# Kernel tuning notes

Hardware: AMD Instinct MI355X
Metric: run time of the kernel (lower is better)

Reference implementation:

```python
import jax, jax.numpy as jnp
import numpy as np

B, V, T, F, H = 32, 16, 64, 64, 512
NBINS = 36  # 360 / delta (delta_cog = delta_rb = 10)
OUT = 4     # output_size


def setup_inputs() -> dict:
    key = jax.random.key(0)
    ks = jax.random.split(key, 12)
    s = 1.0 / np.sqrt(H)
    return {
        'sequence': jax.random.normal(ks[0], (B, V, T, F), jnp.float32),
        'dist_matrix': jax.random.uniform(ks[1], (B, V, T, V), jnp.float32),
        'rb_matrix': jax.random.randint(ks[2], (B, V, T, V), 0, NBINS).astype(jnp.int32),
        'cog_matrix': jax.random.randint(ks[3], (B, V, T, V), 0, NBINS).astype(jnp.int32),
        'seq_mask': jnp.ones((B, V, T), jnp.float32),
        'maxval': jax.random.uniform(ks[4], (B, F), jnp.float32) + 1.0,
        'minval': jax.random.uniform(ks[5], (B, F), jnp.float32),
        # per-vessel LSTMCell params (PyTorch gate order i,f,g,o stacked along 4H)
        'W_ih': jax.random.normal(ks[6], (V, 4 * H, F), jnp.float32) * s,
        'W_hh': jax.random.normal(ks[7], (V, 4 * H, H), jnp.float32) * s,
        'b_ih': jnp.zeros((V, 4 * H), jnp.float32),
        'b_hh': jnp.zeros((V, 4 * H), jnp.float32),
        # hardwired attention domain table [360/delta_cog, 360/delta_rb]
        'domain': jax.random.normal(ks[8], (NBINS, NBINS), jnp.float32),
        # per-vessel softAttention linear (2H -> H)
        'soft_W': jax.random.normal(ks[9], (V, H, 2 * H), jnp.float32) * s,
        'soft_b': jnp.zeros((V, H), jnp.float32),
        # shared output linear (H -> F)
        'out_W': jax.random.normal(ks[10], (F, H), jnp.float32) * s,
        'out_b': jnp.zeros((F,), jnp.float32),
    }


def _forward(sequence, dist_matrix, rb_matrix, cog_matrix, seq_mask, maxval, minval,
             W_ih, W_hh, b_ih, b_hh, domain, soft_W, soft_b, out_W, out_b):
    B_, V_, T_, F_ = sequence.shape
    H_ = W_hh.shape[-1]

    def hardwired(h, r, d, m, cg):
        # h: [B,V,H]; r,d,cg: [B,V,V]; m: [B,V]
        mul1 = m[:, :, None] * m[:, None, :]
        mul2 = domain[cg, r]
        w = jax.nn.relu(mul2 - d) * mul1
        w = w / jax.lax.stop_gradient(jnp.max(w))  # torch: weights /= weights.data.max()
        return jnp.einsum('bvw,bwh->bvh', w, h)

    def lstm_step(x, h, c):
        # vectorized over V independent LSTMCells
        g = (jnp.einsum('bvf,vgf->bvg', x, W_ih)
             + jnp.einsum('bvh,vgh->bvg', h, W_hh) + b_ih + b_hh)
        i, f, gg, o = jnp.split(g, 4, axis=-1)
        c_new = jax.nn.sigmoid(f) * c + jax.nn.sigmoid(i) * jnp.tanh(gg)
        h_new = jax.nn.sigmoid(o) * jnp.tanh(c_new)
        return h_new, c_new

    h0 = jnp.zeros((B_, V_, H_), sequence.dtype)
    c0 = jnp.zeros((B_, V_, H_), sequence.dtype)
    xs = (jnp.moveaxis(sequence, 2, 0), jnp.moveaxis(rb_matrix, 2, 0),
          jnp.moveaxis(dist_matrix, 2, 0), jnp.moveaxis(seq_mask, 2, 0),
          jnp.moveaxis(cog_matrix, 2, 0))

    def enc_step(carry, xt):
        h, c = carry
        x, r, d, m, cg = xt
        wh = hardwired(h, r, d, m, cg)
        h, c = lstm_step(x, wh, c)
        return (h, c), h

    (h, c), enc = jax.lax.scan(enc_step, (h0, c0), xs)
    enc = jnp.moveaxis(enc, 0, 2)  # encodedInput [B,V,T,H]

    # decoder, prediction step i=0 (prediction_length=1)
    wh = hardwired(h, rb_matrix[:, :, -1], dist_matrix[:, :, -1],
                   seq_mask[:, :, -1], cog_matrix[:, :, -1])
    # get_previous_sequence: denormalize under no_grad
    prev = jax.lax.stop_gradient(
        sequence[:, :, -1] * (maxval - minval)[:, None, :] + minval[:, None, :])
    h, c = lstm_step(prev, wh, c)

    # per-vessel softAttention
    score = jnp.einsum('bvth,bvh->bvt', enc, h)
    alpha = jax.nn.softmax(score * seq_mask, axis=-1)
    ctx = jnp.einsum('bvt,bvth->bvh', alpha, enc)
    # faithful to torch.stack((ctx, h)).view(B, 2H) memory-reinterpret per vessel
    z = jnp.moveaxis(jnp.stack([ctx, h], axis=0), 2, 0).reshape(V_, B_, 2 * H_)
    h = jnp.moveaxis(
        jnp.tanh(jnp.einsum('vbk,vhk->vbh', z, soft_W) + soft_b[:, None, :]), 0, 1)

    out = jax.nn.relu(jnp.einsum('bvh,fh->bvf', h, out_W) + out_b)
    return out[:, :, None, :OUT]  # [B, V, prediction_length=1, output_size]


def reference(sequence, dist_matrix, rb_matrix, cog_matrix, seq_mask, maxval, minval,
              W_ih, W_hh, b_ih, b_hh, domain, soft_W, soft_b, out_W, out_b,
              maxVessels=V):
    return _forward(sequence, dist_matrix, rb_matrix, cog_matrix, seq_mask,
                    maxval, minval, W_ih, W_hh, b_ih, b_hh, domain,
                    soft_W, soft_b, out_W, out_b)
```

## Files before the change

### kernel.cpp

```cpp
#include <hip/hip_runtime.h>
#include <math.h>

#define B 32
#define V 16
#define T 64
#define F 64
#define H 512
#define NB 36
#define G4H 2048

typedef unsigned short u16;
typedef unsigned long long ull;
typedef __attribute__((ext_vector_type(8))) short bf16x8;
typedef __attribute__((ext_vector_type(4))) float f32x4;

#define OFF_H0     0
#define OFF_H1     262144
#define OFF_C      524288
#define OFF_CNT    786432
#define OFF_WALL   819200
#define OFF_CTX    819200
#define OFF_HSOFT  1081344
#define OFF_WMAX   1343488
#define OFF_WHSTG  1343552
#define OFF_SEQSTG 1605696
#define OFF_WSTG   2670656
#define OFF_ENC    12107840

#define WHP 262144
#define WLDS_BYTES 147456

__device__ __forceinline__ float sigmoidf_(float x) { return 1.0f / (1.0f + __expf(-x)); }

__device__ __forceinline__ u16 f2bf(float f) {
    union { float f; unsigned u; } x; x.f = f;
    unsigned r = x.u + 0x7FFF + ((x.u >> 16) & 1);
    return (u16)(r >> 16);
}
__device__ __forceinline__ float bf2f(u16 u) {
    union { unsigned i; float f; } x; x.i = ((unsigned)u) << 16;
    return x.f;
}
__device__ __forceinline__ f32x4 mfma16(bf16x8 a, bf16x8 b, f32x4 c) {
    return __builtin_amdgcn_mfma_f32_16x16x32_bf16(a, b, c, 0, 0, 0);
}
__device__ __forceinline__ bf16x8 mk_bf16x8(ull lo, ull hi) {
    union { ull u[2]; bf16x8 v; } x; x.u[0] = lo; x.u[1] = hi; return x.v;
}
__device__ __forceinline__ bf16x8 mk_bf16x8q(uint4 q) {
    union { uint4 q; bf16x8 v; } x; x.q = q; return x.v;
}

__device__ __forceinline__ ull ld_agent(const ull* p) {
    return __hip_atomic_load((ull*)p, __ATOMIC_RELAXED, __HIP_MEMORY_SCOPE_AGENT);
}
__device__ __forceinline__ void st_agent(ull* p, ull x) {
    __hip_atomic_store(p, x, __ATOMIC_RELAXED, __HIP_MEMORY_SCOPE_AGENT);
}
__device__ __forceinline__ void st_agent_f(float* p, float x) {
    __hip_atomic_store(p, x, __ATOMIC_RELAXED, __HIP_MEMORY_SCOPE_AGENT);
}
__device__ __forceinline__ void st_agent_u32(unsigned* p, unsigned x) {
    __hip_atomic_store(p, x, __ATOMIC_RELAXED, __HIP_MEMORY_SCOPE_AGENT);
}
__device__ __forceinline__ unsigned ld_agent_u32(const unsigned* p) {
    return __hip_atomic_load((unsigned*)p, __ATOMIC_RELAXED, __HIP_MEMORY_SCOPE_AGENT);
}

#define NZB 3200
#define NHW 64
#define NWC 4608
#define NSS 1040
__global__ __launch_bounds__(256) void k_prep(
    float* __restrict__ ws,
    const float* __restrict__ dist, const int* __restrict__ rb,
    const int* __restrict__ cog, const float* __restrict__ mask,
    const float* __restrict__ domain, float* __restrict__ w_all,
    float* __restrict__ wmax_all,
    const float* __restrict__ W_ih, const float* __restrict__ W_hh,
    u16* __restrict__ Wstg,
    const float* __restrict__ seq, const float* __restrict__ maxval,
    const float* __restrict__ minval, u16* __restrict__ seqstg) {
    __shared__ float red[256];
    int bid = blockIdx.x;
    int tid = threadIdx.x;

    if (bid < NZB) {
        ws[bid * 256 + tid] = 0.0f;
        return;
    }
    if (bid < NZB + NHW) {
        int t = bid - NZB;
        float lmax = 0.0f;
        for (int idx = tid; idx < B * V * V; idx += 256) {
            int b = idx >> 8;
            int rem = idx & 255;
            int i = rem >> 4, j = rem & 15;
            int base = ((b * V + i) * T + t) * V + j;
            float val = domain[cog[base] * NB + rb[base]] - dist[base];
            val = val > 0.0f ? val : 0.0f;
            val *= mask[(b * V + i) * T + t] * mask[(b * V + j) * T + t];
            w_all[t * (B * V * V) + idx] = val;
            lmax = fmaxf(lmax, val);
        }
        red[tid] = lmax;
        __syncthreads();
        for (int s = 128; s > 0; s >>= 1) {
            if (tid < s) red[tid] = fmaxf(red[tid], red[tid + s]);
            __syncthreads();
        }
        if (tid == 0) wmax_all[t] = red[0];
        return;
    }
    if (bid < NZB + NHW + NWC) {
        int idx = bid - (NZB + NHW);
        int v = idx / 288, hk = (idx / 18) & 15, ks = idx % 18;
#pragma unroll
        for (int s = 0; s < 2; ++s) {
            int slot = tid + s * 256;
            int nt = slot >> 6, lane = slot & 63;
            int g = nt >> 1, hh = nt & 1;
            int col = g * H + hk * 32 + hh * 16 + (lane & 15);
            int k = ks * 32 + ((lane >> 4) << 3);
            const float* src = (k < F) ? &W_ih[(v * G4H + col) * F + k]
                                       : &W_hh[(v * G4H + col) * H + (k - F)];
            float4 x0 = *(const float4*)src;
            float4 x1 = *(const float4*)(src + 4);
            union { u16 u[8]; uint4 q; } pk;
            pk.u[0] = f2bf(x0.x); pk.u[1] = f2bf(x0.y); pk.u[2] = f2bf(x0.z); pk.u[3] = f2bf(x0.w);
            pk.u[4] = f2bf(x1.x); pk.u[5] = f2bf(x1.y); pk.u[6] = f2bf(x1.z); pk.u[7] = f2bf(x1.w);
            *(uint4*)&Wstg[(size_t)((((v * 16 + hk) * 18 + ks) * 8 + nt) * 64 + lane) * 8] = pk.q;
        }
        return;
    }
    {
        int idx = bid - (NZB + NHW + NWC);
        int v = idx / 65, t = idx % 65;
        int mt = tid >> 7, ks = (tid >> 6) & 1, lane = tid & 63;
        int b = mt * 16 + (lane & 15);
        int f = ks * 32 + ((lane >> 4) << 3);
        union { u16 u[8]; uint4 q; } pk;
        if (t < T) {
            const float* sp = &seq[((b * V + v) * T + t) * F + f];
            float4 x0 = *(const float4*)sp, x1 = *(const float4*)(sp + 4);
            pk.u[0] = f2bf(x0.x); pk.u[1] = f2bf(x0.y); pk.u[2] = f2bf(x0.z); pk.u[3] = f2bf(x0.w);
            pk.u[4] = f2bf(x1.x); pk.u[5] = f2bf(x1.y); pk.u[6] = f2bf(x1.z); pk.u[7] = f2bf(x1.w);
        } else {
            const float* sp = &seq[((b * V + v) * T + (T - 1)) * F + f];
            float4 x0 = *(const float4*)sp, x1 = *(const float4*)(sp + 4);
            float4 mx0 = *(const float4*)&maxval[b * F + f], mx1 = *(const float4*)&maxval[b * F + f + 4];
            float4 mn0 = *(const float4*)&minval[b * F + f], mn1 = *(const float4*)&minval[b * F + f + 4];
            pk.u[0] = f2bf(x0.x * (mx0.x - mn0.x) + mn0.x);
            pk.u[1] = f2bf(x0.y * (mx0.y - mn0.y) + mn0.y);
            pk.u[2] = f2bf(x0.z * (mx0.z - mn0.z) + mn0.z);
            pk.u[3] = f2bf(x0.w * (mx0.w - mn0.w) + mn0.w);
            pk.u[4] = f2bf(x1.x * (mx1.x - mn1.x) + mn1.x);
            pk.u[5] = f2bf(x1.y * (mx1.y - mn1.y) + mn1.y);
            pk.u[6] = f2bf(x1.z * (mx1.z - mn1.z) + mn1.z);
            pk.u[7] = f2bf(x1.w * (mx1.w - mn1.w) + mn1.w);
        }
        *(uint4*)&seqstg[(((size_t)(t * 16 + v)) * 4 + mt * 2 + ks) * 512 + lane * 8] = pk.q;
    }
}

__global__ __launch_bounds__(256) void k_recur(
    const u16* __restrict__ seqstg, const u16* __restrict__ Wstg,
    const float* __restrict__ w_all, const float* __restrict__ wmax_all,
    const float* __restrict__ b_ih, const float* __restrict__ b_hh,
    float* __restrict__ h0buf, float* __restrict__ h1buf,
    float* __restrict__ c, u16* __restrict__ enc, u16* __restrict__ whstg,
    unsigned* __restrict__ bar) {
    extern __shared__ u16 Wlds[];

    int bid = blockIdx.x;
    int v = bid & 15, hk = bid >> 4;
    int tid = threadIdx.x;

    {
        const uint4* wsrc = (const uint4*)(Wstg + (size_t)((v * 16 + hk) * 18) * 4096);
        uint4* wdst = (uint4*)Wlds;
        for (int i = tid; i < 9216; i += 256) wdst[i] = wsrc[i];
    }

    int lane = tid & 63, wvi = tid >> 6;
    int mtw = wvi & 1, hh = wvi >> 1;
    int col = hk * 32 + hh * 16 + (lane & 15);
    int q4 = (lane >> 4) << 2;
    float bi = b_ih[v * G4H + col] + b_hh[v * G4H + col];
    float bf_ = b_ih[v * G4H + H + col] + b_hh[v * G4H + H + col];
    float bg_ = b_ih[v * G4H + 2 * H + col] + b_hh[v * G4H + 2 * H + col];
    float bo = b_ih[v * G4H + 3 * H + col] + b_hh[v * G4H + 3 * H + col];

    unsigned* aslot = bar + (v * 16 + hk) * 16;
    unsigned* bslot = bar + (256 + hk * 16 + v) * 16;
    unsigned* apoll = bar + (v * 16 + (tid & 15)) * 16;
    unsigned* bpoll = bar + (256 + hk * 16 + (tid & 15)) * 16;

    int a_b = tid >> 3;
    int a_cq = tid & 7;
    const int wh_idx = ((((v * 2 + (a_b >> 4)) * 16 + hk) * 64 +
                         (((a_cq >> 1) << 4) + (a_b & 15))) * 8 + (a_cq & 1) * 4);

    __syncthreads();

    for (int t = 0; t <= T; ++t) {
        int par = t & 1;
        int tm = t < T ? t : (T - 1);
        const float* hin = (t & 1) ? h0buf : h1buf;
        float* hout = (t & 1) ? h1buf : h0buf;

        uint4 s0 = *(const uint4*)&seqstg[(((size_t)(t * 16 + v)) * 4 + mtw * 2 + 0) * 512 + lane * 8];
        uint4 s1 = *(const uint4*)&seqstg[(((size_t)(t * 16 + v)) * 4 + mtw * 2 + 1) * 512 + lane * 8];
        float inv = 1.0f / wmax_all[tm];
        const float* wrow = &w_all[(size_t)tm * (B * V * V) + (a_b * V + v) * V];
        float4 wr0 = *(const float4*)(wrow);
        float4 wr1 = *(const float4*)(wrow + 4);
        float4 wr2 = *(const float4*)(wrow + 8);
        float4 wr3 = *(const float4*)(wrow + 12);
        float cprev[4];
#pragma unroll
        for (int r = 0; r < 4; ++r)
            cprev[r] = c[((mtw * 16 + q4 + r) * V + v) * H + col];

        f32x4 acc[4];
        acc[0][0] = bi;  acc[0][1] = bi;  acc[0][2] = bi;  acc[0][3] = bi;
        acc[1][0] = bf_; acc[1][1] = bf_; acc[1][2] = bf_; acc[1][3] = bf_;
        acc[2][0] = bg_; acc[2][1] = bg_; acc[2][2] = bg_; acc[2][3] = bg_;
        acc[3][0] = bo;  acc[3][1] = bo;  acc[3][2] = bo;  acc[3][3] = bo;
        {
            bf16x8 a0f = mk_bf16x8q(s0);
            bf16x8 a1f = mk_bf16x8q(s1);
#pragma unroll
            for (int g = 0; g < 4; ++g)
                acc[g] = mfma16(a0f, *(const bf16x8*)&Wlds[(0 * 8 + (g * 2 + hh)) * 512 + lane * 8], acc[g]);
#pragma unroll
            for (int g = 0; g < 4; ++g)
                acc[g] = mfma16(a1f, *(const bf16x8*)&Wlds[(1 * 8 + (g * 2 + hh)) * 512 + lane * 8], acc[g]);
        }

        if (t > 0) {
            if (tid < 16) {
                while (ld_agent_u32(bpoll) < (unsigned)t) __builtin_amdgcn_s_sleep(1);
            }
            __syncthreads();
        }

        {
            const ull* hb = (const ull*)&hin[(a_b * V) * H + hk * 32 + a_cq * 4];
            float a0 = 0.f, a1 = 0.f, a2 = 0.f, a3 = 0.f;
            const float wj[16] = {wr0.x, wr0.y, wr0.z, wr0.w, wr1.x, wr1.y, wr1.z, wr1.w,
                                  wr2.x, wr2.y, wr2.z, wr2.w, wr3.x, wr3.y, wr3.z, wr3.w};
#pragma unroll
            for (int j = 0; j < 16; ++j) {
                ull lo = ld_agent(hb + (size_t)j * (H / 2));
                ull hi = ld_agent(hb + (size_t)j * (H / 2) + 1);
                union { ull u; float f[2]; } u0, u1;
                u0.u = lo; u1.u = hi;
                a0 = fmaf(wj[j], u0.f[0], a0);
                a1 = fmaf(wj[j], u0.f[1], a1);
                a2 = fmaf(wj[j], u1.f[0], a2);
                a3 = fmaf(wj[j], u1.f[1], a3);
            }
            union { u16 u[4]; ull q; } pk;
            pk.u[0] = f2bf(a0 * inv); pk.u[1] = f2bf(a1 * inv);
            pk.u[2] = f2bf(a2 * inv); pk.u[3] = f2bf(a3 * inv);
            st_agent((ull*)&whstg[par * WHP + wh_idx], pk.q);
        }
        __syncthreads();
        if (tid == 0) st_agent_u32(aslot, (unsigned)(t + 1));

        if (tid < 16) {
            while (ld_agent_u32(apoll) < (unsigned)(t + 1)) __builtin_amdgcn_s_sleep(1);
        }
        __syncthreads();

        bf16x8 afr[16];
#pragma unroll
        for (int ksw = 0; ksw < 16; ++ksw) {
            const ull* src = (const ull*)&whstg[par * WHP + (((v * 2 + mtw) * 16 + ksw) * 64 + lane) * 8];
            ull lo = ld_agent(src), hi = ld_agent(src + 1);
            afr[ksw] = mk_bf16x8(lo, hi);
        }
#pragma unroll
        for (int ks = 0; ks < 16; ++ks) {
#pragma unroll
            for (int g = 0; g < 4; ++g) {
                bf16x8 wfr = *(const bf16x8*)&Wlds[((ks + 2) * 8 + (g * 2 + hh)) * 512 + lane * 8];
                acc[g] = mfma16(afr[ks], wfr, acc[g]);
            }
        }

        float cnv[4], hnv[4];
#pragma unroll
        for (int r = 0; r < 4; ++r) {
            float gi = acc[0][r];
            float gf = acc[1][r];
            float gg = acc[2][r];
            float go = acc[3][r];
            cnv[r] = sigmoidf_(gf) * cprev[r] + sigmoidf_(gi) * tanhf(gg);
            hnv[r] = sigmoidf_(go) * tanhf(cnv[r]);
            int b = mtw * 16 + q4 + r;
            st_agent_f(&hout[(b * V + v) * H + col], hnv[r]);
        }
        if (t < T) {
            __syncthreads();
            if (tid == 0) st_agent_u32(bslot, (unsigned)(t + 1));
        }

#pragma unroll
        for (int r = 0; r < 4; ++r) {
            int b = mtw * 16 + q4 + r;
            c[(b * V + v) * H + col] = cnv[r];
            if (t < T) enc[((size_t)(b * V + v) * T + t) * H + col] = f2bf(hnv[r]);
        }
    }
}

__global__ __launch_bounds__(256) void k_attn(
    const u16* __restrict__ enc, const float* __restrict__ h,
    const float* __restrict__ mask, float* __restrict__ ctx) {
    int bid = blockIdx.x;
    int b = bid >> 4, v = bid & 15;
    int tid = threadIdx.x;
    int wave = tid >> 6, lane = tid & 63;
    __shared__ float hs[H];
    __shared__ float sc[T];
    __shared__ float al[T];
    const u16* encbase = enc + (size_t)((b * V + v) * T) * H;
    const float* hb = h + (b * V + v) * H;
    for (int i = tid; i < H; i += 256) hs[i] = hb[i];
    __syncthreads();
    for (int tt = wave; tt < T; tt += 4) {
        const u16* e = encbase + tt * H;
        float p = 0.0f;
#pragma unroll
        for (int ii = 0; ii < 8; ++ii) p += bf2f(e[ii * 64 + lane]) * hs[ii * 64 + lane];
        for (int off = 32; off; off >>= 1) p += __shfl_down(p, off, 64);
        if (lane == 0) sc[tt] = p;
    }
    __syncthreads();
    if (tid < 64) {
        float m_t = mask[(b * V + v) * T + tid];
        float s = sc[tid] * m_t;
        float mx = s;
        for (int off = 32; off; off >>= 1) mx = fmaxf(mx, __shfl_xor(mx, off, 64));
        float e = __expf(s - mx);
        float sum = e;
        for (int off = 32; off; off >>= 1) sum += __shfl_xor(sum, off, 64);
        al[tid] = e / sum;
    }
    __syncthreads();
    for (int hh = tid; hh < H; hh += 256) {
        float a = 0.0f;
        for (int tt = 0; tt < T; ++tt) a += al[tt] * bf2f(encbase[tt * H + hh]);
        ctx[(b * V + v) * H + hh] = a;
    }
}

__global__ __launch_bounds__(256) void k_soft(
    const float* __restrict__ ctx, const float* __restrict__ hdec,
    const float* __restrict__ soft_W, const float* __restrict__ soft_b,
    float* __restrict__ hsoft) {
    int v = blockIdx.x;
    int h0 = blockIdx.y * 32;
    int tid = threadIdx.x;
    int cg = tid & 31, rg = tid >> 5;
    __shared__ float sA[32][36];
    __shared__ float sW2[32][36];
    float* sAf = &sA[0][0];
    float* sWf = &sW2[0][0];
    float acc[4] = {0.f, 0.f, 0.f, 0.f};
    int arow = tid >> 3, akq = tid & 7;
    float4 areg, wreg;

    {
        int k = akq * 4;
        const float* src = (arow < 16) ? ctx : hdec;
        int bsrc = 2 * (arow & 15) + (k >= H ? 1 : 0);
        areg = *(const float4*)&src[(bsrc * V + v) * H + (k & (H - 1))];
        wreg = *(const float4*)&soft_W[(v * H + h0 + arow) * (2 * H) + k];
    }
    for (int kc = 0; kc < 2 * H; kc += 32) {
        __syncthreads();
        *(float4*)&sAf[arow * 36 + akq * 4] = areg;
        *(float4*)&sWf[arow * 36 + akq * 4] = wreg;
        __syncthreads();
        if (kc + 32 < 2 * H) {
            int k = kc + 32 + akq * 4;
            const float* src = (arow < 16) ? ctx : hdec;
            int bsrc = 2 * (arow & 15) + (k >= H ? 1 : 0);
            areg = *(const float4*)&src[(bsrc * V + v) * H + (k & (H - 1))];
            wreg = *(const float4*)&soft_W[(v * H + h0 + arow) * (2 * H) + kc + 32 + akq * 4];
        }
#pragma unroll
        for (int k4 = 0; k4 < 8; ++k4) {
            float4 wv = *(const float4*)&sWf[cg * 36 + k4 * 4];
            float4 a0 = *(const float4*)&sAf[(rg * 4 + 0) * 36 + k4 * 4];
            float4 a1 = *(const float4*)&sAf[(rg * 4 + 1) * 36 + k4 * 4];
            float4 a2 = *(const float4*)&sAf[(rg * 4 + 2) * 36 + k4 * 4];
            float4 a3 = *(const float4*)&sAf[(rg * 4 + 3) * 36 + k4 * 4];
            acc[0] += a0.x * wv.x + a0.y * wv.y + a0.z * wv.z + a0.w * wv.w;
            acc[1] += a1.x * wv.x + a1.y * wv.y + a1.z * wv.z + a1.w * wv.w;
            acc[2] += a2.x * wv.x + a2.y * wv.y + a2.z * wv.z + a2.w * wv.w;
            acc[3] += a3.x * wv.x + a3.y * wv.y + a3.z * wv.z + a3.w * wv.w;
        }
    }
    float bb = soft_b[v * H + h0 + cg];
#pragma unroll
    for (int r = 0; r < 4; ++r) {
        int row = rg * 4 + r;
        hsoft[(row * V + v) * H + h0 + cg] = tanhf(acc[r] + bb);
    }
}

__global__ __launch_bounds__(64) void k_out(
    const float* __restrict__ hsoft, const float* __restrict__ outW,
    const float* __restrict__ outb, float* __restrict__ out) {
    int bid = blockIdx.x;
    int b = bid >> 4, v = bid & 15;
    int lane = threadIdx.x;
    const float* hb = hsoft + (b * V + v) * H;
    float p[4] = {0.0f, 0.0f, 0.0f, 0.0f};
#pragma unroll
    for (int ii = 0; ii < 8; ++ii) {
        float hv = hb[ii * 64 + lane];
#pragma unroll
        for (int o = 0; o < 4; ++o) p[o] += hv * outW[o * H + ii * 64 + lane];
    }
#pragma unroll
    for (int o = 0; o < 4; ++o) {
        float s = p[o];
        for (int off = 32; off; off >>= 1) s += __shfl_down(s, off, 64);
        if (lane == 0) {
            float val = s + outb[o];
            out[(b * V + v) * 4 + o] = val > 0.0f ? val : 0.0f;
        }
    }
}

extern "C" void kernel_launch(void* const* d_in, const int* in_sizes, int n_in,
                              void* d_out, int out_size, void* d_ws, size_t ws_size,
                              hipStream_t stream) {
    const float* seq = (const float*)d_in[0];
    const float* dist = (const float*)d_in[1];
    const int* rb = (const int*)d_in[2];
    const int* cog = (const int*)d_in[3];
    const float* mask = (const float*)d_in[4];
    const float* maxval = (const float*)d_in[5];
    const float* minval = (const float*)d_in[6];
    const float* W_ih = (const float*)d_in[7];
    const float* W_hh = (const float*)d_in[8];
    const float* b_ih = (const float*)d_in[9];
    const float* b_hh = (const float*)d_in[10];
    const float* domain = (const float*)d_in[11];
    const float* soft_W = (const float*)d_in[12];
    const float* soft_b = (const float*)d_in[13];
    const float* out_W = (const float*)d_in[14];
    const float* out_b = (const float*)d_in[15];

    float* ws = (float*)d_ws;
    float* h0buf = ws + OFF_H0;
    float* h1buf = ws + OFF_H1;
    float* c = ws + OFF_C;
    unsigned* bar = (unsigned*)(ws + OFF_CNT);
    float* w_all = ws + OFF_WALL;
    float* ctx = ws + OFF_CTX;
    float* hsoft = ws + OFF_HSOFT;
    float* wmax_all = ws + OFF_WMAX;
    u16* whstg = (u16*)(ws + OFF_WHSTG);
    u16* seqstg = (u16*)(ws + OFF_SEQSTG);
    u16* Wstg = (u16*)(ws + OFF_WSTG);
    u16* enc = (u16*)(ws + OFF_ENC);

    (void)hipFuncSetAttribute((const void*)k_recur,
                              hipFuncAttributeMaxDynamicSharedMemorySize, WLDS_BYTES);

    k_prep<<<NZB + NHW + NWC + NSS, 256, 0, stream>>>(
        ws, dist, rb, cog, mask, domain, w_all, wmax_all,
        W_ih, W_hh, Wstg, seq, maxval, minval, seqstg);

    k_recur<<<256, 256, WLDS_BYTES, stream>>>(seqstg, Wstg, w_all, wmax_all,
                                              b_ih, b_hh, h0buf, h1buf, c, enc,
                                              whstg, bar);

    k_attn<<<B * V, 256, 0, stream>>>(enc, h0buf, mask, ctx);
    k_soft<<<dim3(16, 16), 256, 0, stream>>>(ctx, h0buf, soft_W, soft_b, hsoft);
    k_out<<<B * V, 64, 0, stream>>>(hsoft, out_W, out_b, (float*)d_out);
}
```

Before: 700.8 us.

## Fuse attention, soft-attention linear and output head into persistent recurrent kernel

Merges the attention, softAttention linear and output-projection kernels into the persistent recurrence kernel. Flag-based grid barriers in workspace replace the kernel boundaries, and agent-scope atomic loads and stores make cross-block data visible. This removes three launches and their tail gaps. It adds spin waits, and the enc writes become 16-bit atomic stores, which may cost bandwidth in the recurrence loop.

```diff
diff --git a/kernel.cpp b/kernel.cpp
--- a/kernel.cpp
+++ b/kernel.cpp
@@ -58,6 +58,9 @@
     __hip_atomic_store(p, x, __ATOMIC_RELAXED, __HIP_MEMORY_SCOPE_AGENT);
 }
 __device__ __forceinline__ void st_agent_f(float* p, float x) {
+    __hip_atomic_store(p, x, __ATOMIC_RELAXED, __HIP_MEMORY_SCOPE_AGENT);
+}
+__device__ __forceinline__ void st_agent_u16(u16* p, u16 x) {
     __hip_atomic_store(p, x, __ATOMIC_RELAXED, __HIP_MEMORY_SCOPE_AGENT);
 }
 __device__ __forceinline__ void st_agent_u32(unsigned* p, unsigned x) {
@@ -163,14 +166,22 @@
     }
 }
 
-__global__ __launch_bounds__(256) void k_recur(
+__global__ __launch_bounds__(256) void k_main(
     const u16* __restrict__ seqstg, const u16* __restrict__ Wstg,
     const float* __restrict__ w_all, const float* __restrict__ wmax_all,
     const float* __restrict__ b_ih, const float* __restrict__ b_hh,
     float* __restrict__ h0buf, float* __restrict__ h1buf,
     float* __restrict__ c, u16* __restrict__ enc, u16* __restrict__ whstg,
-    unsigned* __restrict__ bar) {
+    unsigned* __restrict__ bar,
+    const float* __restrict__ mask, const float* __restrict__ soft_W,
+    const float* __restrict__ soft_b, const float* __restrict__ out_W,
+    const float* __restrict__ out_b, float* __restrict__ ctx,
+    float* __restrict__ hsoft, float* __restrict__ out) {
     extern __shared__ u16 Wlds[];
+    __shared__ float hs[H];
+    __shared__ float scal[2 * T];
+    __shared__ float sA[32][36];
+    __shared__ float sW2[32][36];
 
     int bid = blockIdx.x;
     int v = bid & 15, hk = bid >> 4;
@@ -311,129 +322,169 @@
         for (int r = 0; r < 4; ++r) {
             int b = mtw * 16 + q4 + r;
             c[(b * V + v) * H + col] = cnv[r];
-            if (t < T) enc[((size_t)(b * V + v) * T + t) * H + col] = f2bf(hnv[r]);
-        }
-    }
-}
-
-__global__ __launch_bounds__(256) void k_attn(
-    const u16* __restrict__ enc, const float* __restrict__ h,
-    const float* __restrict__ mask, float* __restrict__ ctx) {
-    int bid = blockIdx.x;
-    int b = bid >> 4, v = bid & 15;
-    int tid = threadIdx.x;
-    int wave = tid >> 6, lane = tid & 63;
-    __shared__ float hs[H];
-    __shared__ float sc[T];
-    __shared__ float al[T];
-    const u16* encbase = enc + (size_t)((b * V + v) * T) * H;
-    const float* hb = h + (b * V + v) * H;
-    for (int i = tid; i < H; i += 256) hs[i] = hb[i];
+            if (t < T) st_agent_u16(&enc[((size_t)(b * V + v) * T + t) * H + col], f2bf(hnv[r]));
+        }
+    }
+
     __syncthreads();
-    for (int tt = wave; tt < T; tt += 4) {
-        const u16* e = encbase + tt * H;
-        float p = 0.0f;
-#pragma unroll
-        for (int ii = 0; ii < 8; ++ii) p += bf2f(e[ii * 64 + lane]) * hs[ii * 64 + lane];
-        for (int off = 32; off; off >>= 1) p += __shfl_down(p, off, 64);
-        if (lane == 0) sc[tt] = p;
+    if (tid == 0) st_agent_u32(bar + (512 + bid) * 16, 1u);
+    {
+        const unsigned* rs = bar + (512 + tid) * 16;
+        while (ld_agent_u32(rs) < 1u) __builtin_amdgcn_s_sleep(1);
     }
     __syncthreads();
-    if (tid < 64) {
-        float m_t = mask[(b * V + v) * T + tid];
-        float s = sc[tid] * m_t;
-        float mx = s;
-        for (int off = 32; off; off >>= 1) mx = fmaxf(mx, __shfl_xor(mx, off, 64));
-        float e = __expf(s - mx);
-        float sum = e;
-        for (int off = 32; off; off >>= 1) sum += __shfl_xor(sum, off, 64);
-        al[tid] = e / sum;
+
+    for (int u = 0; u < 2; ++u) {
+        int ab = (bid >> 4) + u * 16;
+        int av = bid & 15;
+        const u16* encb = enc + ((size_t)(ab * V + av) * T) * H;
+        {
+            ull x = ld_agent((const ull*)(h0buf + (ab * V + av) * H) + tid);
+            union { ull u; float f[2]; } q; q.u = x;
+            hs[tid * 2] = q.f[0]; hs[tid * 2 + 1] = q.f[1];
+        }
+        __syncthreads();
+        for (int tt = wvi; tt < T; tt += 4) {
+            const ull* ep = (const ull*)(encb + tt * H + lane * 8);
+            ull lo = ld_agent(ep), hi = ld_agent(ep + 1);
+            union { ull u; u16 s[4]; } x0, x1; x0.u = lo; x1.u = hi;
+            const float* hq = &hs[lane * 8];
+            float p = bf2f(x0.s[0]) * hq[0] + bf2f(x0.s[1]) * hq[1]
+                    + bf2f(x0.s[2]) * hq[2] + bf2f(x0.s[3]) * hq[3]
+                    + bf2f(x1.s[0]) * hq[4] + bf2f(x1.s[1]) * hq[5]
+                    + bf2f(x1.s[2]) * hq[6] + bf2f(x1.s[3]) * hq[7];
+            for (int off = 32; off; off >>= 1) p += __shfl_down(p, off, 64);
+            if (lane == 0) scal[tt] = p;
+        }
+        __syncthreads();
+        if (tid < 64) {
+            float m_t = mask[(ab * V + av) * T + tid];
+            float s = scal[tid] * m_t;
+            float mx = s;
+            for (int off = 32; off; off >>= 1) mx = fmaxf(mx, __shfl_xor(mx, off, 64));
+            float e = __expf(s - mx);
+            float sum = e;
+            for (int off = 32; off; off >>= 1) sum += __shfl_xor(sum, off, 64);
+            scal[T + tid] = e / sum;
+        }
+        __syncthreads();
+        if (tid < 128) {
+            float a0 = 0.f, a1 = 0.f, a2 = 0.f, a3 = 0.f;
+            for (int tt = 0; tt < T; ++tt) {
+                ull x = ld_agent((const ull*)(encb + tt * H + tid * 4));
+                union { ull u; u16 s[4]; } q; q.u = x;
+                float al = scal[T + tt];
+                a0 = fmaf(al, bf2f(q.s[0]), a0);
+                a1 = fmaf(al, bf2f(q.s[1]), a1);
+                a2 = fmaf(al, bf2f(q.s[2]), a2);
+                a3 = fmaf(al, bf2f(q.s[3]), a3);
+            }
+            float* cp = ctx + (ab * V + av) * H + tid * 4;
+            union { float f[2]; ull u; } q0, q1;
+            q0.f[0] = a0; q0.f[1] = a1; q1.f[0] = a2; q1.f[1] = a3;
+            st_agent((ull*)cp, q0.u);
+            st_agent((ull*)cp + 1, q1.u);
+        }
+        __syncthreads();
     }
     __syncthreads();
-    for (int hh = tid; hh < H; hh += 256) {
-        float a = 0.0f;
-        for (int tt = 0; tt < T; ++tt) a += al[tt] * bf2f(encbase[tt * H + hh]);
-        ctx[(b * V + v) * H + hh] = a;
-    }
-}
-
-__global__ __launch_bounds__(256) void k_soft(
-    const float* __restrict__ ctx, const float* __restrict__ hdec,
-    const float* __restrict__ soft_W, const float* __restrict__ soft_b,
-    float* __restrict__ hsoft) {
-    int v = blockIdx.x;
-    int h0 = blockIdx.y * 32;
-    int tid = threadIdx.x;
-    int cg = tid & 31, rg = tid >> 5;
-    __shared__ float sA[32][36];
-    __shared__ float sW2[32][36];
-    float* sAf = &sA[0][0];
-    float* sWf = &sW2[0][0];
-    float acc[4] = {0.f, 0.f, 0.f, 0.f};
-    int arow = tid >> 3, akq = tid & 7;
-    float4 areg, wreg;
+    if (tid == 0) st_agent_u32(bar + (768 + bid) * 16, 1u);
 
     {
-        int k = akq * 4;
-        const float* src = (arow < 16) ? ctx : hdec;
-        int bsrc = 2 * (arow & 15) + (k >= H ? 1 : 0);
-        areg = *(const float4*)&src[(bsrc * V + v) * H + (k & (H - 1))];
-        wreg = *(const float4*)&soft_W[(v * H + h0 + arow) * (2 * H) + k];
-    }
-    for (int kc = 0; kc < 2 * H; kc += 32) {
-        __syncthreads();
-        *(float4*)&sAf[arow * 36 + akq * 4] = areg;
-        *(float4*)&sWf[arow * 36 + akq * 4] = wreg;
-        __syncthreads();
-        if (kc + 32 < 2 * H) {
-            int k = kc + 32 + akq * 4;
-            const float* src = (arow < 16) ? ctx : hdec;
+        int sv = bid & 15;
+        int h0 = (bid >> 4) * 32;
+        if (tid < 16) {
+            const unsigned* cs = bar + (768 + tid * 16 + sv) * 16;
+            while (ld_agent_u32(cs) < 1u) __builtin_amdgcn_s_sleep(1);
+        }
+        __syncthreads();
+
+        int cg = tid & 31, rg = tid >> 5;
+        float* sAf = &sA[0][0];
+        float* sWf = &sW2[0][0];
+        float accs[4] = {0.f, 0.f, 0.f, 0.f};
+        int arow = tid >> 3, akq = tid & 7;
+        float4 areg, wreg;
+        {
+            int k = akq * 4;
+            const float* src = (arow < 16) ? ctx : h0buf;
             int bsrc = 2 * (arow & 15) + (k >= H ? 1 : 0);
-            areg = *(const float4*)&src[(bsrc * V + v) * H + (k & (H - 1))];
-            wreg = *(const float4*)&soft_W[(v * H + h0 + arow) * (2 * H) + kc + 32 + akq * 4];
-        }
-#pragma unroll
-        for (int k4 = 0; k4 < 8; ++k4) {
-            float4 wv = *(const float4*)&sWf[cg * 36 + k4 * 4];
-            float4 a0 = *(const float4*)&sAf[(rg * 4 + 0) * 36 + k4 * 4];
-            float4 a1 = *(const float4*)&sAf[(rg * 4 + 1) * 36 + k4 * 4];
-            float4 a2 = *(const float4*)&sAf[(rg * 4 + 2) * 36 + k4 * 4];
-            float4 a3 = *(const float4*)&sAf[(rg * 4 + 3) * 36 + k4 * 4];
-            acc[0] += a0.x * wv.x + a0.y * wv.y + a0.z * wv.z + a0.w * wv.w;
-            acc[1] += a1.x * wv.x + a1.y * wv.y + a1.z * wv.z + a1.w * wv.w;
-            acc[2] += a2.x * wv.x + a2.y * wv.y + a2.z * wv.z + a2.w * wv.w;
-            acc[3] += a3.x * wv.x + a3.y * wv.y + a3.z * wv.z + a3.w * wv.w;
-        }
-    }
-    float bb = soft_b[v * H + h0 + cg];
-#pragma unroll
-    for (int r = 0; r < 4; ++r) {
-        int row = rg * 4 + r;
-        hsoft[(row * V + v) * H + h0 + cg] = tanhf(acc[r] + bb);
-    }
-}
-
-__global__ __launch_bounds__(64) void k_out(
-    const float* __restrict__ hsoft, const float* __restrict__ outW,
-    const float* __restrict__ outb, float* __restrict__ out) {
-    int bid = blockIdx.x;
-    int b = bid >> 4, v = bid & 15;
-    int lane = threadIdx.x;
-    const float* hb = hsoft + (b * V + v) * H;
-    float p[4] = {0.0f, 0.0f, 0.0f, 0.0f};
-#pragma unroll
-    for (int ii = 0; ii < 8; ++ii) {
-        float hv = hb[ii * 64 + lane];
-#pragma unroll
-        for (int o = 0; o < 4; ++o) p[o] += hv * outW[o * H + ii * 64 + lane];
-    }
-#pragma unroll
-    for (int o = 0; o < 4; ++o) {
-        float s = p[o];
-        for (int off = 32; off; off >>= 1) s += __shfl_down(s, off, 64);
-        if (lane == 0) {
-            float val = s + outb[o];
-            out[(b * V + v) * 4 + o] = val > 0.0f ? val : 0.0f;
+            const float* sp = &src[(bsrc * V + sv) * H + (k & (H - 1))];
+            ull l0 = ld_agent((const ull*)sp), l1 = ld_agent((const ull*)sp + 1);
+            union { ull u[2]; float4 f; } q; q.u[0] = l0; q.u[1] = l1;
+            areg = q.f;
+            wreg = *(const float4*)&soft_W[(sv * H + h0 + arow) * (2 * H) + k];
+        }
+        for (int kc = 0; kc < 2 * H; kc += 32) {
+            __syncthreads();
+            *(float4*)&sAf[arow * 36 + akq * 4] = areg;
+            *(float4*)&sWf[arow * 36 + akq * 4] = wreg;
+            __syncthreads();
+            if (kc + 32 < 2 * H) {
+                int k = kc + 32 + akq * 4;
+                const float* src = (arow < 16) ? ctx : h0buf;
+                int bsrc = 2 * (arow & 15) + (k >= H ? 1 : 0);
+                const float* sp = &src[(bsrc * V + sv) * H + (k & (H - 1))];
+                ull l0 = ld_agent((const ull*)sp), l1 = ld_agent((const ull*)sp + 1);
+                union { ull u[2]; float4 f; } q; q.u[0] = l0; q.u[1] = l1;
+                areg = q.f;
+                wreg = *(const float4*)&soft_W[(sv * H + h0 + arow) * (2 * H) + kc + 32 + akq * 4];
+            }
+#pragma unroll
+            for (int k4 = 0; k4 < 8; ++k4) {
+                float4 wv = *(const float4*)&sWf[cg * 36 + k4 * 4];
+                float4 a0 = *(const float4*)&sAf[(rg * 4 + 0) * 36 + k4 * 4];
+                float4 a1 = *(const float4*)&sAf[(rg * 4 + 1) * 36 + k4 * 4];
+                float4 a2 = *(const float4*)&sAf[(rg * 4 + 2) * 36 + k4 * 4];
+                float4 a3 = *(const float4*)&sAf[(rg * 4 + 3) * 36 + k4 * 4];
+                accs[0] += a0.x * wv.x + a0.y * wv.y + a0.z * wv.z + a0.w * wv.w;
+                accs[1] += a1.x * wv.x + a1.y * wv.y + a1.z * wv.z + a1.w * wv.w;
+                accs[2] += a2.x * wv.x + a2.y * wv.y + a2.z * wv.z + a2.w * wv.w;
+                accs[3] += a3.x * wv.x + a3.y * wv.y + a3.z * wv.z + a3.w * wv.w;
+            }
+        }
+        float bb = soft_b[sv * H + h0 + cg];
+#pragma unroll
+        for (int r = 0; r < 4; ++r) {
+            int row = rg * 4 + r;
+            st_agent_f(&hsoft[(row * V + sv) * H + h0 + cg], tanhf(accs[r] + bb));
+        }
+    }
+    __syncthreads();
+    if (tid == 0) st_agent_u32(bar + (1024 + bid) * 16, 1u);
+
+    {
+        int ov = bid & 15;
+        if (tid < 16) {
+            const unsigned* ss = bar + (1024 + tid * 16 + ov) * 16;
+            while (ld_agent_u32(ss) < 1u) __builtin_amdgcn_s_sleep(1);
+        }
+        __syncthreads();
+        if (wvi < 2) {
+            int ob = (bid >> 4) + wvi * 16;
+            const float* hbp = hsoft + (ob * V + ov) * H + lane * 8;
+            ull q0 = ld_agent((const ull*)hbp);
+            ull q1 = ld_agent((const ull*)hbp + 1);
+            ull q2 = ld_agent((const ull*)hbp + 2);
+            ull q3 = ld_agent((const ull*)hbp + 3);
+            union { ull u[4]; float f[8]; } hv;
+            hv.u[0] = q0; hv.u[1] = q1; hv.u[2] = q2; hv.u[3] = q3;
+            float p[4] = {0.f, 0.f, 0.f, 0.f};
+#pragma unroll
+            for (int o = 0; o < 4; ++o) {
+                const float* wp = &out_W[o * H + lane * 8];
+#pragma unroll
+                for (int j = 0; j < 8; ++j) p[o] += hv.f[j] * wp[j];
+            }
+#pragma unroll
+            for (int o = 0; o < 4; ++o) {
+                float s = p[o];
+                for (int off = 32; off; off >>= 1) s += __shfl_down(s, off, 64);
+                if (lane == 0) {
+                    float val = s + out_b[o];
+                    out[(ob * V + ov) * 4 + o] = val > 0.0f ? val : 0.0f;
+                }
+            }
         }
     }
 }
@@ -472,18 +523,16 @@
     u16* Wstg = (u16*)(ws + OFF_WSTG);
     u16* enc = (u16*)(ws + OFF_ENC);
 
-    (void)hipFuncSetAttribute((const void*)k_recur,
+    (void)hipFuncSetAttribute((const void*)k_main,
                               hipFuncAttributeMaxDynamicSharedMemorySize, WLDS_BYTES);
 
     k_prep<<<NZB + NHW + NWC + NSS, 256, 0, stream>>>(
         ws, dist, rb, cog, mask, domain, w_all, wmax_all,
         W_ih, W_hh, Wstg, seq, maxval, minval, seqstg);
 
-    k_recur<<<256, 256, WLDS_BYTES, stream>>>(seqstg, Wstg, w_all, wmax_all,
-                                              b_ih, b_hh, h0buf, h1buf, c, enc,
-                                              whstg, bar);
-
-    k_attn<<<B * V, 256, 0, stream>>>(enc, h0buf, mask, ctx);
-    k_soft<<<dim3(16, 16), 256, 0, stream>>>(ctx, h0buf, soft_W, soft_b, hsoft);
-    k_out<<<B * V, 64, 0, stream>>>(hsoft, out_W, out_b, (float*)d_out);
-}
+    k_main<<<256, 256, WLDS_BYTES, stream>>>(seqstg, Wstg, w_all, wmax_all,
+                                             b_ih, b_hh, h0buf, h1buf, c, enc,
+                                             whstg, bar, mask, soft_W, soft_b,
+                                             out_W, out_b, ctx, hsoft,
+                                             (float*)d_out);
+}
```

New measurement: 856.6 us. +22.2%, slower.
